# Kernel tuning notes

Measured on AMD Instinct MI355X. Metric: run time of the kernel, lower is better.

Reference implementation:

```python
import jax, jax.numpy as jnp
import numpy as np

EMBED_DIM = 1024
NUM_HEADS = 16
HEAD_DIM = EMBED_DIM // NUM_HEADS  # 64
MLP_DIM = 4096
EPS = 1e-5  # torch LayerNorm default


def layer_norm(x, gamma, beta):
    mu = jnp.mean(x, axis=-1, keepdims=True)
    var = jnp.mean(jnp.square(x - mu), axis=-1, keepdims=True)
    return (x - mu) * jax.lax.rsqrt(var + EPS) * gamma + beta


def setup_inputs() -> dict:
    key = jax.random.key(0)
    ks = jax.random.split(key, 12)
    s = 0.02
    x = jax.random.normal(ks[0], (2, 2048, EMBED_DIM), dtype=jnp.float32)
    # per-head qkv projections (Linear(embed_dim, 3*head_dim, bias=False)), stacked over heads
    w_qkv = s * jax.random.normal(ks[1], (NUM_HEADS, EMBED_DIM, 3 * HEAD_DIM), dtype=jnp.float32)
    # per-head output proj (Linear(head_dim, head_dim), with bias)
    w_hproj = s * jax.random.normal(ks[2], (NUM_HEADS, HEAD_DIM, HEAD_DIM), dtype=jnp.float32)
    b_hproj = jnp.zeros((NUM_HEADS, HEAD_DIM), dtype=jnp.float32)
    # MHA final proj (Linear(num_heads*head_dim, embed_dim))
    w_out = s * jax.random.normal(ks[3], (NUM_HEADS * HEAD_DIM, EMBED_DIM), dtype=jnp.float32)
    b_out = jnp.zeros((EMBED_DIM,), dtype=jnp.float32)
    # MLP
    w_fc1 = s * jax.random.normal(ks[4], (EMBED_DIM, MLP_DIM), dtype=jnp.float32)
    b_fc1 = jnp.zeros((MLP_DIM,), dtype=jnp.float32)
    w_fc2 = s * jax.random.normal(ks[5], (MLP_DIM, EMBED_DIM), dtype=jnp.float32)
    b_fc2 = jnp.zeros((EMBED_DIM,), dtype=jnp.float32)
    # layer norms
    g1 = jnp.ones((EMBED_DIM,), dtype=jnp.float32)
    be1 = jnp.zeros((EMBED_DIM,), dtype=jnp.float32)
    g2 = jnp.ones((EMBED_DIM,), dtype=jnp.float32)
    be2 = jnp.zeros((EMBED_DIM,), dtype=jnp.float32)
    return dict(x=x, w_qkv=w_qkv, w_hproj=w_hproj, b_hproj=b_hproj,
                w_out=w_out, b_out=b_out, w_fc1=w_fc1, b_fc1=b_fc1,
                w_fc2=w_fc2, b_fc2=b_fc2, g1=g1, be1=be1, g2=g2, be2=be2)


def reference(x, w_qkv, w_hproj, b_hproj, w_out, b_out,
              w_fc1, b_fc1, w_fc2, b_fc2, g1, be1, g2, be2):
    B, S, D = x.shape
    scale = HEAD_DIM ** (-0.5)

    # ---- MSA branch (pre-norm, dropouts are identity at eval) ----
    xn = layer_norm(x, g1, be1)
    qkv = jnp.einsum('bsd,hdf->bhsf', xn, w_qkv)  # [B,H,S,3*hd]
    q, k, v = jnp.split(qkv, 3, axis=-1)           # each [B,H,S,hd]
    attn = jax.nn.softmax(jnp.einsum('bhsd,bhtd->bhst', q, k) * scale, axis=-1)
    o = jnp.einsum('bhst,bhtd->bhsd', attn, v)     # [B,H,S,hd]
    o = jnp.einsum('bhsd,hde->bhse', o, w_hproj) + b_hproj[None, :, None, :]
    # concat heads along last dim (head 0 first), then final proj
    o = o.transpose(0, 2, 1, 3).reshape(B, S, NUM_HEADS * HEAD_DIM)
    o = o @ w_out + b_out
    x = x + o

    # ---- MLP branch ----
    xn = layer_norm(x, g2, be2)
    h = jax.nn.gelu(xn @ w_fc1 + b_fc1, approximate=False)
    x = x + (h @ w_fc2 + b_fc2)
    return x
```

## Files before the change

kernel.cpp:

```cpp
#include <hip/hip_runtime.h>
#include <hip/hip_bf16.h>
#include <math.h>

#define DEV __device__ __forceinline__

typedef float f32x4 __attribute__((ext_vector_type(4)));
typedef short bf16x8 __attribute__((ext_vector_type(8)));

DEV unsigned short f2bf(float f) {
  union { float f; unsigned int u; } c; c.f = f;
  return (unsigned short)((c.u + 0x7FFF + ((c.u >> 16) & 1)) >> 16);
}
DEV float bf2f(unsigned short u) {
  union { unsigned int u; float f; } c; c.u = ((unsigned int)u) << 16;
  return c.f;
}

#define ASYNC_LD16(gp, lp)                                                     \
  __builtin_amdgcn_global_load_lds(                                            \
      (const __attribute__((address_space(1))) void*)(gp),                     \
      (__attribute__((address_space(3))) void*)(lp), 16, 0, 0)

__global__ void trans_f32_bf16(const float* __restrict__ in, unsigned short* __restrict__ out,
                               int R, int C, long inBatch, long outBatch) {
  __shared__ float tile[64][65];
  int ct = blockIdx.x, rt = blockIdx.y, z = blockIdx.z;
  const float* src = in + (long)z * inBatch + (long)rt * 64 * C + ct * 64;
  unsigned short* dst = out + (long)z * outBatch + (long)ct * 64 * R + rt * 64;
  int t = threadIdx.x, c = t & 63, r0 = t >> 6;
#pragma unroll
  for (int i = 0; i < 16; i++) {
    int r = i * 4 + r0;
    tile[r][c] = src[(long)r * C + c];
  }
  __syncthreads();
#pragma unroll
  for (int i = 0; i < 16; i++) {
    int r = i * 4 + r0;
    dst[(long)r * R + c] = f2bf(tile[c][r]);
  }
}

__global__ void combine_wout(const float* __restrict__ w_hproj, const float* __restrict__ w_out,
                             unsigned short* __restrict__ wcombt) {
  int hd = blockIdx.x;
  int h = hd >> 6, d = hd & 63;
  for (int i = 0; i < 4; i++) {
    int e = threadIdx.x + i * 256;
    float acc = 0.f;
    for (int dp = 0; dp < 64; dp++)
      acc += w_hproj[(h * 64 + d) * 64 + dp] * w_out[(h * 64 + dp) * 1024 + e];
    wcombt[(long)e * 1024 + hd] = f2bf(acc);
  }
}

__global__ void combine_bias(const float* __restrict__ b_hproj, const float* __restrict__ w_out,
                             const float* __restrict__ b_out, float* __restrict__ bcomb) {
  __shared__ float part[8][32];
  int e = blockIdx.x * 32 + (threadIdx.x & 31);
  int ks = threadIdx.x >> 5;
  float acc = 0.f;
  for (int k = ks * 128; k < ks * 128 + 128; k++) acc += b_hproj[k] * w_out[(long)k * 1024 + e];
  part[ks][threadIdx.x & 31] = acc;
  __syncthreads();
  if (threadIdx.x < 32) {
    float s = b_out[e];
#pragma unroll
    for (int i = 0; i < 8; i++) s += part[i][threadIdx.x];
    bcomb[e] = s;
  }
}

__global__ void transpose_v(const unsigned short* __restrict__ in, unsigned short* __restrict__ out) {
  __shared__ unsigned short tile[64][65];
  int st = blockIdx.x, bh = blockIdx.y;
  const unsigned short* src = in + (long)bh * 131072 + (long)st * 64 * 64;
  unsigned short* dst = out + (long)bh * 131072 + (long)st * 64;
  int t = threadIdx.x, c = t & 63, r0 = t >> 6;
#pragma unroll
  for (int i = 0; i < 16; i++) tile[i * 4 + r0][c] = src[(i * 4 + r0) * 64 + c];
  __syncthreads();
  int kb = c >> 4, g = kb >> 1, sub = kb & 1, hi2 = (c >> 2) & 3, jj = c & 3;
  int pos = g * 32 + hi2 * 8 + sub * 4 + jj;
#pragma unroll
  for (int i = 0; i < 16; i++) {
    int d = i * 4 + r0;
    dst[(long)d * 2048 + pos] = tile[c][d];
  }
}

__launch_bounds__(256)
__global__ void ln_kernel(const float* __restrict__ x, const float* __restrict__ g,
                          const float* __restrict__ b, unsigned short* __restrict__ out) {
  int row = blockIdx.x, t = threadIdx.x;
  float4 v = ((const float4*)(x + (long)row * 1024))[t];
  float s = v.x + v.y + v.z + v.w;
  float s2 = v.x * v.x + v.y * v.y + v.z * v.z + v.w * v.w;
  for (int o = 32; o; o >>= 1) { s += __shfl_down(s, o); s2 += __shfl_down(s2, o); }
  __shared__ float red[8];
  int w = t >> 6, l = t & 63;
  if (l == 0) { red[w] = s; red[w + 4] = s2; }
  __syncthreads();
  s = red[0] + red[1] + red[2] + red[3];
  s2 = red[4] + red[5] + red[6] + red[7];
  float mu = s * (1.f / 1024.f);
  float var = s2 * (1.f / 1024.f) - mu * mu;
  float rs = rsqrtf(var + 1e-5f);
  float4 gv = ((const float4*)g)[t];
  float4 bv = ((const float4*)b)[t];
  ushort4 o4;
  o4.x = f2bf((v.x - mu) * rs * gv.x + bv.x);
  o4.y = f2bf((v.y - mu) * rs * gv.y + bv.y);
  o4.z = f2bf((v.z - mu) * rs * gv.z + bv.z);
  o4.w = f2bf((v.w - mu) * rs * gv.w + bv.w);
  ((ushort4*)(out + (long)row * 1024))[t] = o4;
}

template <int NP, int ACCUM>
__launch_bounds__(256)
__global__ void reduce_add(const unsigned short* __restrict__ p0,
                           const unsigned short* __restrict__ p1,
                           const unsigned short* __restrict__ p2,
                           const unsigned short* __restrict__ p3,
                           const float* __restrict__ bias, const float* __restrict__ resid,
                           float* __restrict__ out) {
  int i = blockIdx.x * 256 + threadIdx.x;
  float4 b = ((const float4*)bias)[i & 255];
  float4 r = ACCUM ? ((const float4*)out)[i] : ((const float4*)resid)[i];
  float4 o;
  ushort4 a0 = ((const ushort4*)p0)[i];
  ushort4 a1 = ((const ushort4*)p1)[i];
  o.x = r.x + b.x + bf2f(a0.x) + bf2f(a1.x);
  o.y = r.y + b.y + bf2f(a0.y) + bf2f(a1.y);
  o.z = r.z + b.z + bf2f(a0.z) + bf2f(a1.z);
  o.w = r.w + b.w + bf2f(a0.w) + bf2f(a1.w);
  if (NP > 2) {
    ushort4 a2 = ((const ushort4*)p2)[i];
    o.x += bf2f(a2.x); o.y += bf2f(a2.y); o.z += bf2f(a2.z); o.w += bf2f(a2.w);
  }
  if (NP > 3) {
    ushort4 a3 = ((const ushort4*)p3)[i];
    o.x += bf2f(a3.x); o.y += bf2f(a3.y); o.z += bf2f(a3.z); o.w += bf2f(a3.w);
  }
  ((float4*)out)[i] = o;
}

#define EPI_QKV 0
#define EPI_GELU 2
#define EPI_PARTIAL 3

template <int EPI, int BM>
__launch_bounds__(512, 2)
__global__ void gemm256(const unsigned short* __restrict__ A, const unsigned short* __restrict__ Bt,
                        int N, int K, const float* __restrict__ bias,
                        unsigned short* __restrict__ outb,
                        unsigned short* __restrict__ qb, unsigned short* __restrict__ kb,
                        unsigned short* __restrict__ vb,
                        unsigned short* __restrict__ pp0, unsigned short* __restrict__ pp1) {
  constexpr int MR = BM / 32;
  __shared__ alignas(16) unsigned short lds_a[2][BM * 64];
  __shared__ alignas(16) unsigned short lds_b[2][256 * 64];
  int gx = gridDim.x, nwg = gx * gridDim.y;
  int orig = blockIdx.y * gx + blockIdx.x;
  int cpx = nwg >> 3;
  int wg = (orig & 7) * cpx + (orig >> 3);
  int bm = wg % gx, bn = wg / gx;

  int tt = K >> 6, Z = gridDim.z, z = blockIdx.z;
  int bq = tt / Z, rem = tt - bq * Z;
  int nk = bq + (z < rem ? 1 : 0);
  int kt0 = z * bq + (z < rem ? z : rem);

  int t = threadIdx.x, w = t >> 6, l = t & 63;
  int wm = w >> 2, wn = w & 3;
  int lr = l & 15, hi = l >> 4;

  f32x4 acc[MR][4];
  const f32x4 z4 = {0.f, 0.f, 0.f, 0.f};
#pragma unroll
  for (int m = 0; m < MR; m++)
#pragma unroll
    for (int n = 0; n < 4; n++) acc[m][n] = z4;

#define GSTAGE(buf, kt)                                                        \
  do {                                                                         \
    _Pragma("unroll")                                                          \
    for (int i = 0; i < BM / 64; i++) {                   \
      int ch = i * 512 + t;                                                    \
      int row = ch >> 3, cs = ch & 7;                                          \
      int csz = cs ^ (row & 7);                                                \
      ASYNC_LD16(A + (long)(bm * BM + row) * K + (kt0 + (kt)) * 64 + csz * 8,  \
                 lds_a[buf] + (size_t)ch * 8);                                 \
    }                                                                          \
    _Pragma("unroll")                                                          \
    for (int i = 0; i < 4; i++) {                        \
      int ch = i * 512 + t;                                                    \
      int row = ch >> 3, cs = ch & 7;                                          \
      int csz = cs ^ (row & 7);                                                \
      ASYNC_LD16(Bt + (long)(bn * 256 + row) * K + (kt0 + (kt)) * 64 + csz * 8,\
                 lds_b[buf] + (size_t)ch * 8);                                 \
    }                                                                          \
  } while (0)

  GSTAGE(0, 0);
  asm volatile("s_waitcnt vmcnt(0)" ::: "memory");
  asm volatile("s_barrier" ::: "memory");

  for (int kt = 0; kt < nk; ++kt) {
    int cur = kt & 1;
    if (kt + 1 < nk) GSTAGE(cur ^ 1, kt + 1);
#pragma unroll
    for (int kc = 0; kc < 2; kc++) {
      bf16x8 af[MR], bfr[4];
#pragma unroll
      for (int m = 0; m < MR; m++) {
        int row = wm * (BM / 2) + m * 16 + lr;
        af[m] = *(const bf16x8*)((const char*)lds_a[cur] + row * 128 +
                                 ((((kc << 2) | hi) ^ (row & 7)) << 4));
      }
#pragma unroll
      for (int n = 0; n < 4; n++) {
        int row = wn * 64 + n * 16 + lr;
        bfr[n] = *(const bf16x8*)((const char*)lds_b[cur] + row * 128 +
                                  ((((kc << 2) | hi) ^ (row & 7)) << 4));
      }
      __builtin_amdgcn_s_setprio(1);
#pragma unroll
      for (int m = 0; m < MR; m++)
#pragma unroll
        for (int n = 0; n < 4; n++)
          acc[m][n] = __builtin_amdgcn_mfma_f32_16x16x32_bf16(af[m], bfr[n], acc[m][n], 0, 0, 0);
      __builtin_amdgcn_s_setprio(0);
    }
    if (kt + 1 < nk) {
      asm volatile("s_waitcnt vmcnt(0)" ::: "memory");
      asm volatile("s_barrier" ::: "memory");
    }
  }
#undef GSTAGE

#pragma unroll
  for (int m = 0; m < MR; m++) {
#pragma unroll
    for (int n = 0; n < 4; n++) {
      int c = bn * 256 + wn * 64 + n * 16 + lr;
#pragma unroll
      for (int j = 0; j < 4; j++) {
        int r = bm * BM + wm * (BM / 2) + m * 16 + hi * 4 + j;
        float val = acc[m][n][j];
        if (EPI == EPI_QKV) {
          int h = c / 192, f = c - h * 192;
          int part = f >> 6, d = f & 63;
          int b = r >> 11, s = r & 2047;
          long idx = ((long)(b * 16 + h) * 2048 + s) * 64 + d;
          if (part == 0) qb[idx] = f2bf(val * 0.18033688011112042f);
          else if (part == 1) kb[idx] = f2bf(val);
          else vb[idx] = f2bf(val);
        } else if (EPI == EPI_GELU) {
          float u = val + bias[c];
          float z2 = u * (0.7978845608f + 0.0356774081f * u * u) * 2.885390082f;
          float e2 = exp2f(z2);
          float th = 1.f - 2.f / (e2 + 1.f);
          outb[(long)r * N + c] = f2bf(0.5f * u * (1.f + th));
        } else {
          unsigned short* pd = (z == 0) ? pp0 : pp1;
          pd[(long)r * N + c] = f2bf(val);
        }
      }
    }
  }
}

__launch_bounds__(256)
__global__ void attn_kernel(const unsigned short* __restrict__ Qg,
                            const unsigned short* __restrict__ Kg,
                            const unsigned short* __restrict__ Vt,
                            unsigned short* __restrict__ Og) {
  __shared__ alignas(16) unsigned short k_lds[2][64 * 64];
  __shared__ alignas(16) unsigned short v_lds[2][64 * 64];
  int orig = blockIdx.y * 32 + blockIdx.x;
  int wg = (orig & 7) * 128 + (orig >> 3);
  int qt = wg & 31, bh = wg >> 5;

  int t = threadIdx.x, w = t >> 6, l = t & 63, lr = l & 15, hi = l >> 4;
  const unsigned short* Qh = Qg + (long)bh * 131072;
  const char* Kh = (const char*)(Kg + (long)bh * 131072);
  const char* Vh = (const char*)(Vt + (long)bh * 131072);

  int qrow = qt * 64 + w * 16 + lr;
  bf16x8 qf0 = *(const bf16x8*)(Qh + (long)qrow * 64 + hi * 8);
  bf16x8 qf1 = *(const bf16x8*)(Qh + (long)qrow * 64 + 32 + hi * 8);
  asm volatile("" :: "v"(qf0), "v"(qf1));

  const f32x4 z4 = {0.f, 0.f, 0.f, 0.f};
  f32x4 accO[4];
#pragma unroll
  for (int j = 0; j < 4; j++) accO[j] = z4;
  float m_q = -1e30f, lsum = 0.f;

#define STAGE(b, kt)                                                           \
  do {                                                                         \
    _Pragma("unroll")                                                          \
    for (int i = 0; i < 2; i++) {                                              \
      int o = (t + i * 256) * 16;                                              \
      int row = o >> 7;                                                        \
      int colb = (o & 127) ^ ((row & 7) << 4);                                 \
      ASYNC_LD16(Kh + (long)((kt) * 64 + row) * 128 + colb,                    \
                 (char*)k_lds[b] + (w * 64 + i * 256) * 16);                   \
      ASYNC_LD16(Vh + (long)row * 4096 + (kt) * 128 + colb,                    \
                 (char*)v_lds[b] + (w * 64 + i * 256) * 16);                   \
    }                                                                          \
  } while (0)

  STAGE(0, 0);

  for (int kt = 0; kt < 32; ++kt) {
    int cur = kt & 1;
    if (kt < 31) {
      STAGE(cur ^ 1, kt + 1);
      asm volatile("s_waitcnt vmcnt(4)" ::: "memory");
    } else {
      asm volatile("s_waitcnt vmcnt(0)" ::: "memory");
    }
    __builtin_amdgcn_s_barrier();

    f32x4 sacc[4];
#pragma unroll
    for (int kbk = 0; kbk < 4; kbk++) sacc[kbk] = z4;
    __builtin_amdgcn_s_setprio(1);
#pragma unroll
    for (int kbk = 0; kbk < 4; kbk++) {
      int krow = kbk * 16 + lr;
      int sw = (krow & 7) << 4;
      const char* kbase = (const char*)k_lds[cur] + krow * 128;
      bf16x8 kf0 = *(const bf16x8*)(kbase + ((hi * 16) ^ sw));
      bf16x8 kf1 = *(const bf16x8*)(kbase + ((64 + hi * 16) ^ sw));
      sacc[kbk] = __builtin_amdgcn_mfma_f32_16x16x32_bf16(kf0, qf0, sacc[kbk], 0, 0, 0);
      sacc[kbk] = __builtin_amdgcn_mfma_f32_16x16x32_bf16(kf1, qf1, sacc[kbk], 0, 0, 0);
    }
    __builtin_amdgcn_s_setprio(0);

    float mx = -1e30f;
#pragma unroll
    for (int kbk = 0; kbk < 4; kbk++)
#pragma unroll
      for (int r = 0; r < 4; r++) mx = fmaxf(mx, sacc[kbk][r]);
    mx = fmaxf(mx, __shfl_xor(mx, 16));
    mx = fmaxf(mx, __shfl_xor(mx, 32));
    if (!__all(mx <= m_q + 8.f)) {
      float mnew = fmaxf(m_q, mx);
      float fac = exp2f(m_q - mnew);
      m_q = mnew;
      lsum *= fac;
      float fj[4];
#pragma unroll
      for (int j = 0; j < 4; j++) fj[j] = __shfl(fac, ((l >> 4) << 2) | j);
#pragma unroll
      for (int db = 0; db < 4; db++)
#pragma unroll
        for (int j = 0; j < 4; j++) accO[db][j] *= fj[j];
    }
    float rs = 0.f;
#pragma unroll
    for (int kbk = 0; kbk < 4; kbk++)
#pragma unroll
      for (int r = 0; r < 4; r++) {
        float p = exp2f(sacc[kbk][r] - m_q);
        sacc[kbk][r] = p;
        rs += p;
      }
    rs += __shfl_xor(rs, 16);
    rs += __shfl_xor(rs, 32);
    lsum += rs;

    bf16x8 pa0, pa1;
#pragma unroll
    for (int r = 0; r < 4; r++) {
      pa0[r] = (short)f2bf(sacc[0][r]);
      pa0[r + 4] = (short)f2bf(sacc[1][r]);
      pa1[r] = (short)f2bf(sacc[2][r]);
      pa1[r + 4] = (short)f2bf(sacc[3][r]);
    }

    __builtin_amdgcn_s_setprio(1);
#pragma unroll
    for (int g = 0; g < 2; g++) {
      bf16x8 pf = g ? pa1 : pa0;
#pragma unroll
      for (int db = 0; db < 4; db++) {
        int d = db * 16 + lr;
        int sw = (d & 7) << 4;
        bf16x8 vf = *(const bf16x8*)((const char*)v_lds[cur] + d * 128 + ((g * 64 + hi * 16) ^ sw));
        accO[db] = __builtin_amdgcn_mfma_f32_16x16x32_bf16(pf, vf, accO[db], 0, 0, 0);
      }
    }
    __builtin_amdgcn_s_setprio(0);

    if (kt < 31) {
      asm volatile("s_waitcnt lgkmcnt(0)" ::: "memory");
      __builtin_amdgcn_s_barrier();
    }
  }
#undef STAGE

  float linv[4];
#pragma unroll
  for (int j = 0; j < 4; j++) linv[j] = 1.f / __shfl(lsum, ((l >> 4) << 2) | j);

  int b = bh >> 4, h = bh & 15;
#pragma unroll
  for (int db = 0; db < 4; db++)
#pragma unroll
    for (int j = 0; j < 4; j++) {
      int s = qt * 64 + w * 16 + hi * 4 + j;
      Og[((long)(b * 2048 + s)) * 1024 + h * 64 + db * 16 + lr] = f2bf(accO[db][j] * linv[j]);
    }
}

extern "C" void kernel_launch(void* const* d_in, const int* in_sizes, int n_in,
                              void* d_out, int out_size, void* d_ws, size_t ws_size,
                              hipStream_t stream) {
  const float* x = (const float*)d_in[0];
  const float* w_qkv = (const float*)d_in[1];
  const float* w_hproj = (const float*)d_in[2];
  const float* b_hproj = (const float*)d_in[3];
  const float* w_out = (const float*)d_in[4];
  const float* b_out = (const float*)d_in[5];
  const float* w_fc1 = (const float*)d_in[6];
  const float* b_fc1 = (const float*)d_in[7];
  const float* w_fc2 = (const float*)d_in[8];
  const float* b_fc2 = (const float*)d_in[9];
  const float* g1 = (const float*)d_in[10];
  const float* be1 = (const float*)d_in[11];
  const float* g2 = (const float*)d_in[12];
  const float* be2 = (const float*)d_in[13];
  float* out = (float*)d_out;

  char* ws = (char*)d_ws;
  unsigned short* wqkvt = (unsigned short*)(ws + 0);
  unsigned short* wfc1t = (unsigned short*)(ws + 6291456);
  unsigned short* wfc2t = (unsigned short*)(ws + 14680064);
  unsigned short* wcombt = (unsigned short*)(ws + 23068672);
  float* bcomb = (float*)(ws + 25165824);
  unsigned short* xn = (unsigned short*)(ws + 25169920);
  unsigned short* qb = (unsigned short*)(ws + 33558528);
  unsigned short* kb = (unsigned short*)(ws + 41947136);
  unsigned short* vb = (unsigned short*)(ws + 50335744);
  unsigned short* attn_o = (unsigned short*)(ws + 58724352);
  unsigned short* h1 = qb;
  unsigned short* vt = xn;
  unsigned short* f2p0 = wfc1t;
  unsigned short* f2p1 = xn;

  trans_f32_bf16<<<dim3(3, 16, 16), 256, 0, stream>>>(w_qkv, wqkvt, 1024, 192,
                                                      196608L, 196608L);
  trans_f32_bf16<<<dim3(64, 16, 1), 256, 0, stream>>>(w_fc1, wfc1t, 1024, 4096, 0, 0);
  trans_f32_bf16<<<dim3(16, 64, 1), 256, 0, stream>>>(w_fc2, wfc2t, 4096, 1024, 0, 0);
  combine_wout<<<1024, 256, 0, stream>>>(w_hproj, w_out, wcombt);
  combine_bias<<<32, 256, 0, stream>>>(b_hproj, w_out, b_out, bcomb);

  ln_kernel<<<4096, 256, 0, stream>>>(x, g1, be1, xn);
  gemm256<EPI_QKV, 256><<<dim3(16, 12, 1), 512, 0, stream>>>(xn, wqkvt, 3072, 1024,
      nullptr, nullptr, qb, kb, vb, nullptr, nullptr);
  transpose_v<<<dim3(32, 32), 256, 0, stream>>>(vb, vt);
  attn_kernel<<<dim3(32, 32), 256, 0, stream>>>(qb, kb, vt, attn_o);
  gemm256<EPI_PARTIAL, 128><<<dim3(32, 4, 2), 512, 0, stream>>>(attn_o, wcombt, 1024, 1024,
      nullptr, nullptr, nullptr, nullptr, nullptr, qb, kb);
  reduce_add<2, 0><<<4096, 256, 0, stream>>>(qb, kb, nullptr, nullptr, bcomb, x, out);

  ln_kernel<<<4096, 256, 0, stream>>>(out, g2, be2, xn);
  gemm256<EPI_GELU, 256><<<dim3(16, 16, 1), 512, 0, stream>>>(xn, wfc1t, 4096, 1024,
      b_fc1, h1, nullptr, nullptr, nullptr, nullptr, nullptr);
  gemm256<EPI_PARTIAL, 128><<<dim3(32, 4, 2), 512, 0, stream>>>(h1, wfc2t, 1024, 4096,
      nullptr, nullptr, nullptr, nullptr, nullptr, f2p0, f2p1);
  reduce_add<2, 1><<<4096, 256, 0, stream>>>(f2p0, f2p1, nullptr, nullptr, b_fc2, nullptr, out);
}
```

Before: 322.2 us.

## Triple-buffer GEMM K pipeline and use 128-row tiles for all GEMMs

Replaces the double-buffered GEMM with a three-stage LDS ring that prefetches two K tiles ahead, waiting with a partial vmcnt so one stage stays in flight. All GEMMs, including QKV and FC1, now use 128-row M tiles, which doubles those grids. The aim is to hide global-load latency and improve CU coverage. The cost is larger LDS use per block and less operand reuse per tile in the QKV and FC1 GEMMs. The unused NP parameter is removed from reduce_add.

Result: slower. 346.5 us (+7.5%).

```diff
diff --git a/kernel.cpp b/kernel.cpp
--- a/kernel.cpp
+++ b/kernel.cpp
@@ -116,32 +116,22 @@
   ((ushort4*)(out + (long)row * 1024))[t] = o4;
 }
 
-template <int NP, int ACCUM>
+template <int ACCUM>
 __launch_bounds__(256)
 __global__ void reduce_add(const unsigned short* __restrict__ p0,
                            const unsigned short* __restrict__ p1,
-                           const unsigned short* __restrict__ p2,
-                           const unsigned short* __restrict__ p3,
                            const float* __restrict__ bias, const float* __restrict__ resid,
                            float* __restrict__ out) {
   int i = blockIdx.x * 256 + threadIdx.x;
   float4 b = ((const float4*)bias)[i & 255];
   float4 r = ACCUM ? ((const float4*)out)[i] : ((const float4*)resid)[i];
-  float4 o;
   ushort4 a0 = ((const ushort4*)p0)[i];
   ushort4 a1 = ((const ushort4*)p1)[i];
+  float4 o;
   o.x = r.x + b.x + bf2f(a0.x) + bf2f(a1.x);
   o.y = r.y + b.y + bf2f(a0.y) + bf2f(a1.y);
   o.z = r.z + b.z + bf2f(a0.z) + bf2f(a1.z);
   o.w = r.w + b.w + bf2f(a0.w) + bf2f(a1.w);
-  if (NP > 2) {
-    ushort4 a2 = ((const ushort4*)p2)[i];
-    o.x += bf2f(a2.x); o.y += bf2f(a2.y); o.z += bf2f(a2.z); o.w += bf2f(a2.w);
-  }
-  if (NP > 3) {
-    ushort4 a3 = ((const ushort4*)p3)[i];
-    o.x += bf2f(a3.x); o.y += bf2f(a3.y); o.z += bf2f(a3.z); o.w += bf2f(a3.w);
-  }
   ((float4*)out)[i] = o;
 }
 
@@ -149,17 +139,16 @@
 #define EPI_GELU 2
 #define EPI_PARTIAL 3
 
-template <int EPI, int BM>
+template <int EPI>
 __launch_bounds__(512, 2)
-__global__ void gemm256(const unsigned short* __restrict__ A, const unsigned short* __restrict__ Bt,
-                        int N, int K, const float* __restrict__ bias,
-                        unsigned short* __restrict__ outb,
-                        unsigned short* __restrict__ qb, unsigned short* __restrict__ kb,
-                        unsigned short* __restrict__ vb,
-                        unsigned short* __restrict__ pp0, unsigned short* __restrict__ pp1) {
-  constexpr int MR = BM / 32;
-  __shared__ alignas(16) unsigned short lds_a[2][BM * 64];
-  __shared__ alignas(16) unsigned short lds_b[2][256 * 64];
+__global__ void gemm_p(const unsigned short* __restrict__ A, const unsigned short* __restrict__ Bt,
+                       int N, int K, const float* __restrict__ bias,
+                       unsigned short* __restrict__ outb,
+                       unsigned short* __restrict__ qb, unsigned short* __restrict__ kb,
+                       unsigned short* __restrict__ vb,
+                       unsigned short* __restrict__ pp0, unsigned short* __restrict__ pp1) {
+  __shared__ alignas(16) unsigned short lds_a[3][128 * 64];
+  __shared__ alignas(16) unsigned short lds_b[3][256 * 64];
   int gx = gridDim.x, nwg = gx * gridDim.y;
   int orig = blockIdx.y * gx + blockIdx.x;
   int cpx = nwg >> 3;
@@ -175,25 +164,25 @@
   int wm = w >> 2, wn = w & 3;
   int lr = l & 15, hi = l >> 4;
 
-  f32x4 acc[MR][4];
+  f32x4 acc[4][4];
   const f32x4 z4 = {0.f, 0.f, 0.f, 0.f};
 #pragma unroll
-  for (int m = 0; m < MR; m++)
+  for (int m = 0; m < 4; m++)
 #pragma unroll
     for (int n = 0; n < 4; n++) acc[m][n] = z4;
 
 #define GSTAGE(buf, kt)                                                        \
   do {                                                                         \
     _Pragma("unroll")                                                          \
-    for (int i = 0; i < BM / 64; i++) {                   \
+    for (int i = 0; i < 2; i++) {                                              \
       int ch = i * 512 + t;                                                    \
       int row = ch >> 3, cs = ch & 7;                                          \
       int csz = cs ^ (row & 7);                                                \
-      ASYNC_LD16(A + (long)(bm * BM + row) * K + (kt0 + (kt)) * 64 + csz * 8,  \
+      ASYNC_LD16(A + (long)(bm * 128 + row) * K + (kt0 + (kt)) * 64 + csz * 8, \
                  lds_a[buf] + (size_t)ch * 8);                                 \
     }                                                                          \
     _Pragma("unroll")                                                          \
-    for (int i = 0; i < 4; i++) {                        \
+    for (int i = 0; i < 4; i++) {                                              \
       int ch = i * 512 + t;                                                    \
       int row = ch >> 3, cs = ch & 7;                                          \
       int csz = cs ^ (row & 7);                                                \
@@ -203,18 +192,19 @@
   } while (0)
 
   GSTAGE(0, 0);
-  asm volatile("s_waitcnt vmcnt(0)" ::: "memory");
+  GSTAGE(1, 1);
+  asm volatile("s_waitcnt vmcnt(6)" ::: "memory");
   asm volatile("s_barrier" ::: "memory");
 
   for (int kt = 0; kt < nk; ++kt) {
-    int cur = kt & 1;
-    if (kt + 1 < nk) GSTAGE(cur ^ 1, kt + 1);
+    int cur = kt % 3;
+    if (kt + 2 < nk) GSTAGE((kt + 2) % 3, kt + 2);
 #pragma unroll
     for (int kc = 0; kc < 2; kc++) {
-      bf16x8 af[MR], bfr[4];
-#pragma unroll
-      for (int m = 0; m < MR; m++) {
-        int row = wm * (BM / 2) + m * 16 + lr;
+      bf16x8 af[4], bfr[4];
+#pragma unroll
+      for (int m = 0; m < 4; m++) {
+        int row = wm * 64 + m * 16 + lr;
         af[m] = *(const bf16x8*)((const char*)lds_a[cur] + row * 128 +
                                  ((((kc << 2) | hi) ^ (row & 7)) << 4));
       }
@@ -226,27 +216,31 @@
       }
       __builtin_amdgcn_s_setprio(1);
 #pragma unroll
-      for (int m = 0; m < MR; m++)
+      for (int m = 0; m < 4; m++)
 #pragma unroll
         for (int n = 0; n < 4; n++)
           acc[m][n] = __builtin_amdgcn_mfma_f32_16x16x32_bf16(af[m], bfr[n], acc[m][n], 0, 0, 0);
       __builtin_amdgcn_s_setprio(0);
     }
     if (kt + 1 < nk) {
-      asm volatile("s_waitcnt vmcnt(0)" ::: "memory");
+      if (kt + 2 < nk) {
+        asm volatile("s_waitcnt vmcnt(6)" ::: "memory");
+      } else {
+        asm volatile("s_waitcnt vmcnt(0)" ::: "memory");
+      }
       asm volatile("s_barrier" ::: "memory");
     }
   }
 #undef GSTAGE
 
 #pragma unroll
-  for (int m = 0; m < MR; m++) {
+  for (int m = 0; m < 4; m++) {
 #pragma unroll
     for (int n = 0; n < 4; n++) {
       int c = bn * 256 + wn * 64 + n * 16 + lr;
 #pragma unroll
       for (int j = 0; j < 4; j++) {
-        int r = bm * BM + wm * (BM / 2) + m * 16 + hi * 4 + j;
+        int r = bm * 128 + wm * 64 + m * 16 + hi * 4 + j;
         float val = acc[m][n][j];
         if (EPI == EPI_QKV) {
           int h = c / 192, f = c - h * 192;
@@ -460,18 +454,18 @@
   combine_bias<<<32, 256, 0, stream>>>(b_hproj, w_out, b_out, bcomb);
 
   ln_kernel<<<4096, 256, 0, stream>>>(x, g1, be1, xn);
-  gemm256<EPI_QKV, 256><<<dim3(16, 12, 1), 512, 0, stream>>>(xn, wqkvt, 3072, 1024,
+  gemm_p<EPI_QKV><<<dim3(32, 12, 1), 512, 0, stream>>>(xn, wqkvt, 3072, 1024,
       nullptr, nullptr, qb, kb, vb, nullptr, nullptr);
   transpose_v<<<dim3(32, 32), 256, 0, stream>>>(vb, vt);
   attn_kernel<<<dim3(32, 32), 256, 0, stream>>>(qb, kb, vt, attn_o);
-  gemm256<EPI_PARTIAL, 128><<<dim3(32, 4, 2), 512, 0, stream>>>(attn_o, wcombt, 1024, 1024,
+  gemm_p<EPI_PARTIAL><<<dim3(32, 4, 2), 512, 0, stream>>>(attn_o, wcombt, 1024, 1024,
       nullptr, nullptr, nullptr, nullptr, nullptr, qb, kb);
-  reduce_add<2, 0><<<4096, 256, 0, stream>>>(qb, kb, nullptr, nullptr, bcomb, x, out);
+  reduce_add<0><<<4096, 256, 0, stream>>>(qb, kb, bcomb, x, out);
 
   ln_kernel<<<4096, 256, 0, stream>>>(out, g2, be2, xn);
-  gemm256<EPI_GELU, 256><<<dim3(16, 16, 1), 512, 0, stream>>>(xn, wfc1t, 4096, 1024,
+  gemm_p<EPI_GELU><<<dim3(32, 16, 1), 512, 0, stream>>>(xn, wfc1t, 4096, 1024,
       b_fc1, h1, nullptr, nullptr, nullptr, nullptr, nullptr);
-  gemm256<EPI_PARTIAL, 128><<<dim3(32, 4, 2), 512, 0, stream>>>(h1, wfc2t, 1024, 4096,
+  gemm_p<EPI_PARTIAL><<<dim3(32, 4, 2), 512, 0, stream>>>(h1, wfc2t, 1024, 4096,
       nullptr, nullptr, nullptr, nullptr, nullptr, f2p0, f2p1);
-  reduce_add<2, 1><<<4096, 256, 0, stream>>>(f2p0, f2p1, nullptr, nullptr, b_fc2, nullptr, out);
-}
+  reduce_add<1><<<4096, 256, 0, stream>>>(f2p0, f2p1, b_fc2, nullptr, out);
+}
```
